# Performance work log

Measured on AMD Instinct MI355X. Metric: run time of the kernel, lower is better.

The kernel has to match this reference:

```python
import jax, jax.numpy as jnp
import numpy as np

N_NODES = 20000
N_EDGES = 320000
N_GRAPHS = 64


def gat_conv(x, src, dst, W, a_src, a_dst, bias, heads, ch, concat):
    # x: [N, F_in]; W: [F_in, heads*ch]; a_src/a_dst: [heads, ch]
    N = x.shape[0]
    h = (x @ W).reshape(N, heads, ch)                       # [N, H, C]
    alpha_s = jnp.sum(h * a_src, axis=-1)                   # [N, H]
    alpha_d = jnp.sum(h * a_dst, axis=-1)                   # [N, H]
    e = jax.nn.leaky_relu(alpha_s[src] + alpha_d[dst], 0.2) # [E, H]
    # segment softmax over incoming edges of each destination node
    m = jax.ops.segment_max(e, dst, num_segments=N)         # [N, H]
    ex = jnp.exp(e - m[dst])
    denom = jax.ops.segment_sum(ex, dst, num_segments=N)    # [N, H]
    alpha = ex / (denom[dst] + 1e-16)                       # [E, H]
    msg = h[src] * alpha[:, :, None]                        # [E, H, C]
    out = jax.ops.segment_sum(msg, dst, num_segments=N)     # [N, H, C]
    out = out.reshape(N, heads * ch) if concat else out.mean(axis=1)
    return out + bias, alpha


def setup_inputs() -> dict:
    key = jax.random.key(0)
    ks = jax.random.split(key, 24)
    dim_in, md, dim_out = 8, 64, 128
    hid = md * 4  # 256
    p = lambda k, shape: jax.random.normal(k, shape, dtype=jnp.float32) * 0.1
    inp = {
        "x_ppi": jax.random.normal(ks[0], (N_NODES, dim_in), dtype=jnp.float32),
        "ppi_edge_index": jax.random.randint(ks[1], (2, N_EDGES), 0, N_NODES),
        "ppi_batch": jnp.sort(jax.random.randint(ks[2], (N_NODES,), 0, N_GRAPHS)),
        # GATConv 1: dim_in -> 64, heads=4, concat
        "W1": p(ks[3], (dim_in, 4 * md)), "a_src1": p(ks[4], (4, md)), "a_dst1": p(ks[5], (4, md)), "b_gat1": jnp.zeros((hid,), jnp.float32),
        "lw1": p(ks[6], (dim_in, hid)), "lb1": jnp.zeros((hid,), jnp.float32),
        # GATConv 2: 256 -> 64, heads=4, concat
        "W2": p(ks[7], (hid, 4 * md)), "a_src2": p(ks[8], (4, md)), "a_dst2": p(ks[9], (4, md)), "b_gat2": jnp.zeros((hid,), jnp.float32),
        "lw2": p(ks[10], (hid, hid)), "lb2": jnp.zeros((hid,), jnp.float32),
        # GATConv 3: 256 -> 128, heads=6, concat=False (mean)
        "W3": p(ks[11], (hid, 6 * dim_out)), "a_src3": p(ks[12], (6, dim_out)), "a_dst3": p(ks[13], (6, dim_out)), "b_gat3": jnp.zeros((dim_out,), jnp.float32),
        "lw3": p(ks[14], (hid, dim_out)), "lb3": jnp.zeros((dim_out,), jnp.float32),
        # BatchNorm1d(dim_out), training-mode batch statistics
        "bn_gamma": jnp.ones((dim_out,), jnp.float32), "bn_beta": jnp.zeros((dim_out,), jnp.float32),
    }
    return inp


def reference(x_ppi, ppi_edge_index, ppi_batch,
              W1, a_src1, a_dst1, b_gat1, lw1, lb1,
              W2, a_src2, a_dst2, b_gat2, lw2, lb2,
              W3, a_src3, a_dst3, b_gat3, lw3, lb3,
              bn_gamma, bn_beta):
    src, dst = ppi_edge_index[0], ppi_edge_index[1]
    g1, _ = gat_conv(x_ppi, src, dst, W1, a_src1, a_dst1, b_gat1, heads=4, ch=64, concat=True)
    x = jax.nn.relu(g1 + x_ppi @ lw1 + lb1)
    g2, _ = gat_conv(x, src, dst, W2, a_src2, a_dst2, b_gat2, heads=4, ch=64, concat=True)
    x = jax.nn.relu(g2 + x @ lw2 + lb2)
    x_res = x @ lw3 + lb3
    g3, att = gat_conv(x, src, dst, W3, a_src3, a_dst3, b_gat3, heads=6, ch=128, concat=False)
    x = g3 + x_res
    x = jax.nn.relu(x)
    # BatchNorm1d, training mode (biased variance, eps=1e-5)
    mu = x.mean(axis=0)
    var = jnp.mean((x - mu) ** 2, axis=0)
    x = (x - mu) * jax.lax.rsqrt(var + 1e-5) * bn_gamma + bn_beta
    # global max pool over graphs
    pooled = jax.ops.segment_max(x, ppi_batch, num_segments=N_GRAPHS)
    return pooled, att
```

## Files before the change

### kernel.cpp

```cpp
#include <hip/hip_runtime.h>
#include <hip/hip_bf16.h>
#include <math.h>

#define N_NODES 20000
#define N_EDGES 320000
#define N_GRAPHS 64

typedef __bf16 bf16_t;
typedef bf16_t bf16x8 __attribute__((ext_vector_type(8)));
typedef bf16_t bf16x4 __attribute__((ext_vector_type(4)));
typedef bf16_t bf16x2 __attribute__((ext_vector_type(2)));
typedef float f32x4 __attribute__((ext_vector_type(4)));
typedef float f32x2 __attribute__((ext_vector_type(2)));

__global__ void hist_k(const int* __restrict__ dst, int* __restrict__ deg, int E) {
    int e = blockIdx.x * 256 + threadIdx.x;
    if (e < E) atomicAdd(&deg[dst[e]], 1);
}

__global__ __launch_bounds__(1024) void scan_k(const int* __restrict__ deg,
                                               int* __restrict__ offs,
                                               int* __restrict__ cursor, int n) {
    __shared__ int s_ws[16];
    int tid = threadIdx.x;
    int lane = tid & 63, w = tid >> 6;
    int carry = 0;
    for (int base = 0; base < n; base += 1024) {
        int i = base + tid;
        int v = (i < n) ? deg[i] : 0;
        int x = v;
        #pragma unroll
        for (int off = 1; off < 64; off <<= 1) {
            int t = __shfl_up(x, off);
            if (lane >= off) x += t;
        }
        if (lane == 63) s_ws[w] = x;
        __syncthreads();
        if (tid < 16) {
            int y = s_ws[tid];
            #pragma unroll
            for (int off = 1; off < 16; off <<= 1) {
                int t = __shfl_up(y, off);
                if (tid >= off) y += t;
            }
            s_ws[tid] = y;
        }
        __syncthreads();
        int wbase = (w > 0) ? s_ws[w - 1] : 0;
        int ex = carry + wbase + x - v;
        if (i < n) { offs[i] = ex; cursor[i] = ex; }
        carry += s_ws[15];
        __syncthreads();
    }
    if (tid == 0) offs[n] = carry;
}

__global__ void scatter_k(const int* __restrict__ src, const int* __restrict__ dst,
                          int* __restrict__ cursor, int* __restrict__ csr_src,
                          int* __restrict__ csr_eid, int E) {
    int e = blockIdx.x * 256 + threadIdx.x;
    if (e < E) {
        int d = dst[e];
        int p = atomicAdd(&cursor[d], 1);
        csr_src[p] = src[e];
        csr_eid[p] = e;
    }
}

__global__ __launch_bounds__(256) void wt_k(const float* __restrict__ W,
                                            bf16_t* __restrict__ Bt, int K, int N) {
    __shared__ float t[32][33];
    int k0 = blockIdx.y * 32, n0 = blockIdx.x * 32;
    int tx = threadIdx.x & 31, ty = threadIdx.x >> 5;
    for (int i = ty; i < 32; i += 8) t[i][tx] = W[(size_t)(k0 + i) * N + n0 + tx];
    __syncthreads();
    for (int i = ty; i < 32; i += 8)
        Bt[(size_t)(n0 + i) * K + k0 + tx] = (bf16_t)t[tx][i];
}

__global__ void w3s_k(const float* __restrict__ W3, const float* __restrict__ lw3,
                      bf16_t* __restrict__ Bt) {
    int id = blockIdx.x * 256 + threadIdx.x;
    if (id >= 128 * 1792) return;
    int n = id / 1792, k = id - n * 1792;
    float v;
    if (k < 1536) {
        int h = k >> 8, c = k & 255;
        v = W3[(size_t)c * 768 + h * 128 + n] * (1.f / 6.f);
    } else {
        int c = k - 1536;
        v = lw3[(size_t)c * 128 + n];
    }
    Bt[id] = (bf16_t)v;
}

__global__ void b40_k(const float* __restrict__ W1, const float* __restrict__ lw1,
                      float* __restrict__ B) {
    int id = blockIdx.x * 256 + threadIdx.x;
    if (id >= 40 * 256) return;
    int k = id >> 8, n = id & 255;
    float v;
    if (k < 32) {
        int h = k >> 3, c = k & 7;
        v = ((n >> 6) == h) ? W1[(size_t)c * 256 + n] : 0.f;
    } else {
        int c = k - 32;
        v = lw1[(size_t)c * 256 + n];
    }
    B[id] = v;
}

__global__ void va_k(const float* __restrict__ W, const float* __restrict__ a_s,
                     const float* __restrict__ a_d, float* __restrict__ Va,
                     float* __restrict__ Vd, int H, int C) {
    int k = blockIdx.x;
    int lane = threadIdx.x;
    const float* wr = W + (size_t)k * H * C;
    for (int h = 0; h < H; ++h) {
        float sa = 0.f, sd = 0.f;
        for (int c = lane; c < C; c += 64) {
            float wv = wr[h * C + c];
            sa += wv * a_s[h * C + c];
            sd += wv * a_d[h * C + c];
        }
        #pragma unroll
        for (int m = 32; m; m >>= 1) { sa += __shfl_xor(sa, m); sd += __shfl_xor(sd, m); }
        if (lane == 0) { Va[k * H + h] = sa; Vd[k * H + h] = sd; }
    }
}

__global__ void addb_k(const float* __restrict__ a, const float* __restrict__ b,
                       float* __restrict__ o, int n) {
    int i = blockIdx.x * 256 + threadIdx.x;
    if (i < n) o[i] = a[i] + b[i];
}

template <typename OUT>
__global__ __launch_bounds__(256) void gemm_k(const float* __restrict__ A,
                                              const float* __restrict__ B,
                                              OUT* __restrict__ C,
                                              const float* __restrict__ bias,
                                              int M, int N, int K, int relu) {
    __shared__ float As[16][65];
    __shared__ float Bs[16][64];
    int tid = threadIdx.x;
    int tx = tid & 15, ty = tid >> 4;
    int row0 = blockIdx.y * 64, col0 = blockIdx.x * 64;
    float acc[4][4] = {};
    for (int k0 = 0; k0 < K; k0 += 16) {
        #pragma unroll
        for (int i = 0; i < 4; ++i) {
            int idx = tid + i * 256;
            int m = idx >> 4, kk = idx & 15;
            int gm = row0 + m, gk = k0 + kk;
            As[kk][m] = (gm < M && gk < K) ? A[(size_t)gm * K + gk] : 0.f;
        }
        #pragma unroll
        for (int i = 0; i < 4; ++i) {
            int idx = tid + i * 256;
            int kk = idx >> 6, n = idx & 63;
            int gk = k0 + kk, gn = col0 + n;
            Bs[kk][n] = (gk < K && gn < N) ? B[(size_t)gk * N + gn] : 0.f;
        }
        __syncthreads();
        #pragma unroll
        for (int kk = 0; kk < 16; ++kk) {
            float a[4], b[4];
            #pragma unroll
            for (int i = 0; i < 4; ++i) a[i] = As[kk][ty * 4 + i];
            #pragma unroll
            for (int j = 0; j < 4; ++j) b[j] = Bs[kk][tx * 4 + j];
            #pragma unroll
            for (int i = 0; i < 4; ++i)
                #pragma unroll
                for (int j = 0; j < 4; ++j) acc[i][j] += a[i] * b[j];
        }
        __syncthreads();
    }
    #pragma unroll
    for (int i = 0; i < 4; ++i) {
        int gm = row0 + ty * 4 + i;
        if (gm >= M) continue;
        #pragma unroll
        for (int j = 0; j < 4; ++j) {
            int gn = col0 + tx * 4 + j;
            if (gn < N) {
                float r = acc[i][j] + (bias ? bias[gn] : 0.f);
                if (relu) r = fmaxf(r, 0.f);
                C[(size_t)gm * N + gn] = (OUT)r;
            }
        }
    }
}

template <typename OUT>
__global__ __launch_bounds__(256) void gemm_bf16_hn_k(
    const bf16_t* __restrict__ A, const bf16_t* __restrict__ Bt,
    OUT* __restrict__ C, const float* __restrict__ bias, int M, int N, int K,
    const float* __restrict__ asv, const float* __restrict__ adv,
    float* __restrict__ as_o, float* __restrict__ ad_o, int H) {
    __shared__ bf16_t As[128][40];
    __shared__ bf16_t Bs[64][40];
    int tid = threadIdx.x;
    int row0 = blockIdx.y * 128, col0 = blockIdx.x * 64;
    int wave = tid >> 6, lane = tid & 63, quad = lane >> 4, l16 = lane & 15;
    f32x4 acc[2][4] = {};
    int sr = tid >> 2;
    int sc = (tid & 3) * 8;
    for (int k0 = 0; k0 < K; k0 += 32) {
        #pragma unroll
        for (int half = 0; half < 2; ++half) {
            int r = sr + half * 64;
            int gm = row0 + r;
            bf16x8 v = {};
            if (gm < M) v = *(const bf16x8*)&A[(size_t)gm * K + k0 + sc];
            *(bf16x8*)&As[r][sc] = v;
        }
        {
            int gn = col0 + sr;
            bf16x8 w = {};
            if (gn < N) w = *(const bf16x8*)&Bt[(size_t)gn * K + k0 + sc];
            *(bf16x8*)&Bs[sr][sc] = w;
        }
        __syncthreads();
        bf16x8 af[2], bfr[4];
        #pragma unroll
        for (int i = 0; i < 2; ++i)
            af[i] = *(const bf16x8*)&As[wave * 32 + i * 16 + l16][quad * 8];
        #pragma unroll
        for (int j = 0; j < 4; ++j)
            bfr[j] = *(const bf16x8*)&Bs[j * 16 + l16][quad * 8];
        #pragma unroll
        for (int i = 0; i < 2; ++i)
            #pragma unroll
            for (int j = 0; j < 4; ++j)
                acc[i][j] = __builtin_amdgcn_mfma_f32_16x16x32_bf16(af[i], bfr[j],
                                                                   acc[i][j], 0, 0, 0);
        __syncthreads();
    }
    #pragma unroll
    for (int i = 0; i < 2; ++i) {
        int base_m = row0 + wave * 32 + i * 16 + quad * 4;
        #pragma unroll
        for (int j = 0; j < 4; ++j) {
            int gn = col0 + j * 16 + l16;
            float bv = bias ? bias[gn] : 0.f;
            #pragma unroll
            for (int r = 0; r < 4; ++r) {
                int gm = base_m + r;
                if (gm < M) C[(size_t)gm * N + gn] = (OUT)(acc[i][j][r] + bv);
            }
        }
    }
    if (asv) {
        int hd = col0 >> 6;
        float av[4], dv[4];
        #pragma unroll
        for (int j = 0; j < 4; ++j) {
            int ca = col0 + j * 16 + l16;
            av[j] = asv[ca];
            dv[j] = adv[ca];
        }
        #pragma unroll
        for (int i = 0; i < 2; ++i) {
            float sp[4] = {}, sd[4] = {};
            #pragma unroll
            for (int j = 0; j < 4; ++j)
                #pragma unroll
                for (int r = 0; r < 4; ++r) {
                    sp[r] += acc[i][j][r] * av[j];
                    sd[r] += acc[i][j][r] * dv[j];
                }
            #pragma unroll
            for (int m = 1; m < 16; m <<= 1)
                #pragma unroll
                for (int r = 0; r < 4; ++r) {
                    sp[r] += __shfl_xor(sp[r], m);
                    sd[r] += __shfl_xor(sd[r], m);
                }
            if (l16 == 0) {
                #pragma unroll
                for (int r = 0; r < 4; ++r) {
                    int gm = row0 + wave * 32 + i * 16 + quad * 4 + r;
                    if (gm < M) {
                        as_o[gm * H + hd] = sp[r];
                        ad_o[gm * H + hd] = sd[r];
                    }
                }
            }
        }
    }
}

__global__ __launch_bounds__(256) void gemm_bf16_thin_k(
    const bf16_t* __restrict__ A, const bf16_t* __restrict__ Bt,
    float* __restrict__ C, const float* __restrict__ bias, int M, int N, int K) {
    __shared__ bf16_t As[32][40];
    __shared__ bf16_t Bs[64][40];
    int tid = threadIdx.x;
    int row0 = blockIdx.y * 32, col0 = blockIdx.x * 64;
    int wave = tid >> 6, lane = tid & 63, quad = lane >> 4, l16 = lane & 15;
    int wr = wave & 1;
    int wc = wave >> 1;
    f32x4 acc[2] = {};
    int ar = tid >> 2, ac = (tid & 3) * 8;
    for (int k0 = 0; k0 < K; k0 += 32) {
        if (tid < 128) {
            int gm = row0 + ar;
            bf16x8 v = {};
            if (gm < M) v = *(const bf16x8*)&A[(size_t)gm * K + k0 + ac];
            *(bf16x8*)&As[ar][ac] = v;
        }
        *(bf16x8*)&Bs[ar][ac] = *(const bf16x8*)&Bt[(size_t)(col0 + ar) * K + k0 + ac];
        __syncthreads();
        bf16x8 af = *(const bf16x8*)&As[wr * 16 + l16][quad * 8];
        #pragma unroll
        for (int j = 0; j < 2; ++j) {
            bf16x8 bf = *(const bf16x8*)&Bs[wc * 32 + j * 16 + l16][quad * 8];
            acc[j] = __builtin_amdgcn_mfma_f32_16x16x32_bf16(af, bf, acc[j], 0, 0, 0);
        }
        __syncthreads();
    }
    #pragma unroll
    for (int j = 0; j < 2; ++j) {
        int gn = col0 + wc * 32 + j * 16 + l16;
        float bv = bias[gn];
        #pragma unroll
        for (int r = 0; r < 4; ++r) {
            int gm = row0 + wr * 16 + quad * 4 + r;
            if (gm < M) C[(size_t)gm * N + gn] = fmaxf(acc[j][r] + bv, 0.f);
        }
    }
}

__device__ __forceinline__ float leaky02(float v) { return v > 0.f ? v : 0.2f * v; }

__global__ void asad1_k(const float* __restrict__ x, const float* __restrict__ Va,
                        const float* __restrict__ Vd, float* __restrict__ as_,
                        float* __restrict__ ad_, int N) {
    int idx = blockIdx.x * 256 + threadIdx.x;
    if (idx >= N * 4) return;
    int j = idx >> 2, h = idx & 3;
    const float* xr = x + (size_t)j * 8;
    float sa = 0.f, sd = 0.f;
    #pragma unroll
    for (int c = 0; c < 8; ++c) {
        sa += xr[c] * Va[c * 4 + h];
        sd += xr[c] * Vd[c * 4 + h];
    }
    as_[idx] = sa;
    ad_[idx] = sd;
}

__global__ void asad3_k(const bf16_t* __restrict__ xb, const float* __restrict__ Va,
                        const float* __restrict__ Vd, float* __restrict__ as_,
                        float* __restrict__ ad_) {
    int j = blockIdx.x;
    int lane = threadIdx.x;
    bf16x4 v = *(const bf16x4*)&xb[(size_t)j * 256 + lane * 4];
    float sa[6] = {}, sd[6] = {};
    #pragma unroll
    for (int i = 0; i < 4; ++i) {
        int k = lane * 4 + i;
        float xv = (float)v[i];
        #pragma unroll
        for (int h = 0; h < 6; ++h) {
            sa[h] += xv * Va[k * 6 + h];
            sd[h] += xv * Vd[k * 6 + h];
        }
    }
    #pragma unroll
    for (int h = 0; h < 6; ++h) {
        float a = sa[h], d = sd[h];
        #pragma unroll
        for (int m = 32; m; m >>= 1) { a += __shfl_xor(a, m); d += __shfl_xor(d, m); }
        if (lane == 0) { as_[j * 6 + h] = a; ad_[j * 6 + h] = d; }
    }
}

__global__ __launch_bounds__(256) void agg_z1_k(
    const float* __restrict__ x, const float* __restrict__ as_,
    const float* __restrict__ ad_, const int* __restrict__ offs,
    const int* __restrict__ csr_src, float* __restrict__ z1) {
    int j = blockIdx.x * 4 + (threadIdx.x >> 6);
    int t = threadIdx.x & 63;
    int e_l = t >> 3, c = t & 7;
    int o0 = offs[j], deg = offs[j + 1] - o0;
    float adj0 = ad_[j * 4 + 0], adj1 = ad_[j * 4 + 1];
    float adj2 = ad_[j * 4 + 2], adj3 = ad_[j * 4 + 3];
    float acc[4] = {}, ws[4] = {};
    for (int e0 = 0; e0 < deg; e0 += 8) {
        int ne = min(8, deg - e0);
        if (e_l < ne) {
            int s = csr_src[o0 + e0 + e_l];
            float xv = x[(size_t)s * 8 + c];
            f32x4 a = *(const f32x4*)&as_[s * 4];
            float w0 = __expf(leaky02(a[0] + adj0));
            float w1 = __expf(leaky02(a[1] + adj1));
            float w2 = __expf(leaky02(a[2] + adj2));
            float w3 = __expf(leaky02(a[3] + adj3));
            acc[0] += w0 * xv; acc[1] += w1 * xv;
            acc[2] += w2 * xv; acc[3] += w3 * xv;
            ws[0] += w0; ws[1] += w1; ws[2] += w2; ws[3] += w3;
        }
    }
    #pragma unroll
    for (int m = 8; m < 64; m <<= 1)
        #pragma unroll
        for (int h = 0; h < 4; ++h) {
            acc[h] += __shfl_xor(acc[h], m);
            ws[h] += __shfl_xor(ws[h], m);
        }
    if (e_l == 0) {
        #pragma unroll
        for (int h = 0; h < 4; ++h)
            z1[(size_t)j * 40 + h * 8 + c] = acc[h] / (ws[h] + 1e-16f);
        z1[(size_t)j * 40 + 32 + c] = x[(size_t)j * 8 + c];
    }
}

__global__ __launch_bounds__(256) void agg_concat_k(
    const bf16_t* __restrict__ h, const float* __restrict__ as_,
    const float* __restrict__ ad_, const int* __restrict__ offs,
    const int* __restrict__ csr_src, const float* __restrict__ lin,
    const float* __restrict__ bgat, bf16_t* __restrict__ xb) {
    int j = blockIdx.x;
    int tid = threadIdx.x;
    int o0 = offs[j], deg = offs[j + 1] - o0;
    __shared__ int s_src[64];
    __shared__ float s_adj[4];
    __shared__ float s_ws[8][4];
    __shared__ float s_inv[4];
    __shared__ float s_red[8][256];
    if (tid < 4) s_adj[tid] = ad_[j * 4 + tid];
    int g = tid >> 5;
    int u = tid & 31;
    int myh = u >> 3;
    const char* hbase = (const char*)h + u * 16;
    f32x4 acc0 = {}, acc1 = {};
    float wsum = 0.f;
    for (int e0 = 0; e0 < deg; e0 += 64) {
        int ne = min(64, deg - e0);
        if (tid < ne) s_src[tid] = csr_src[o0 + e0 + tid];
        __syncthreads();
        float adj = s_adj[myh];
        #pragma unroll 2
        for (int e = g; e < ne; e += 8) {
            int s = s_src[e];
            float w = __expf(leaky02(as_[s * 4 + myh] + adj));
            bf16x8 v = *(const bf16x8*)(hbase + (size_t)s * 512);
            wsum += w;
            #pragma unroll
            for (int i = 0; i < 4; ++i) acc0[i] += w * (float)v[i];
            #pragma unroll
            for (int i = 0; i < 4; ++i) acc1[i] += w * (float)v[4 + i];
        }
        __syncthreads();
    }
    if ((u & 7) == 0) s_ws[g][myh] = wsum;
    *(f32x4*)&s_red[g][u * 8] = acc0;
    *(f32x4*)&s_red[g][u * 8 + 4] = acc1;
    __syncthreads();
    if (tid < 4) {
        float d = 0.f;
        #pragma unroll
        for (int g2 = 0; g2 < 8; ++g2) d += s_ws[g2][tid];
        s_inv[tid] = 1.f / (d + 1e-16f);
    }
    __syncthreads();
    {
        int c = tid;
        float s = 0.f;
        #pragma unroll
        for (int g2 = 0; g2 < 8; ++g2) s += s_red[g2][c];
        float v = fmaxf(s * s_inv[c >> 6] + bgat[c] + lin[(size_t)j * 256 + c], 0.f);
        xb[(size_t)j * 256 + c] = (bf16_t)v;
    }
}

__global__ __launch_bounds__(192) void agg_z3_k(
    const bf16_t* __restrict__ xb, const float* __restrict__ as_,
    const float* __restrict__ ad_, const int* __restrict__ offs,
    const int* __restrict__ csr_src, const int* __restrict__ csr_eid,
    bf16_t* __restrict__ z, float* __restrict__ att) {
    int j = blockIdx.x;
    int tid = threadIdx.x;
    int o0 = offs[j], deg = offs[j + 1] - o0;
    __shared__ float s_adj[6];
    __shared__ int s_src[64];
    __shared__ float s_w[64 * 6];
    __shared__ float s_inv[6];
    if (tid < 6) s_adj[tid] = ad_[j * 6 + tid];
    __syncthreads();
    int h = tid >> 5;
    int c = tid & 31;
    const char* xbase = (const char*)xb + c * 16;
    f32x4 a0 = {}, a1 = {};
    float wsum = 0.f;
    for (int e0 = 0; e0 < deg; e0 += 64) {
        int ne = min(64, deg - e0);
        #pragma unroll
        for (int base = 0; base < 2; ++base) {
            int idx = tid + base * 192;
            if (idx < ne * 6) {
                int e = idx / 6, hh = idx - e * 6;
                int s = csr_src[o0 + e0 + e];
                if (hh == 0) s_src[e] = s;
                s_w[idx] = __expf(leaky02(as_[s * 6 + hh] + s_adj[hh]));
            }
        }
        __syncthreads();
        #pragma unroll 4
        for (int e = 0; e < ne; ++e) {
            int s = s_src[e];
            float w = s_w[e * 6 + h];
            bf16x8 v = *(const bf16x8*)(xbase + (size_t)s * 512);
            wsum += w;
            #pragma unroll
            for (int i = 0; i < 4; ++i) a0[i] += w * (float)v[i];
            #pragma unroll
            for (int i = 0; i < 4; ++i) a1[i] += w * (float)v[4 + i];
        }
        __syncthreads();
    }
    float inv = 1.f / (wsum + 1e-16f);
    {
        bf16x8 o;
        #pragma unroll
        for (int i = 0; i < 4; ++i) o[i] = (bf16_t)(a0[i] * inv);
        #pragma unroll
        for (int i = 0; i < 4; ++i) o[4 + i] = (bf16_t)(a1[i] * inv);
        *(bf16x8*)&z[(size_t)j * 1792 + h * 256 + c * 8] = o;
    }
    if (tid < 32)
        *(bf16x8*)&z[(size_t)j * 1792 + 1536 + tid * 8] =
            *(const bf16x8*)&xb[(size_t)j * 256 + tid * 8];
    if (c == 0) s_inv[h] = inv;
    __syncthreads();
    for (int idx = tid; idx < deg * 6; idx += 192) {
        int e = idx / 6, hh = idx - e * 6;
        int p = o0 + e;
        int s = csr_src[p];
        att[(size_t)csr_eid[p] * 6 + hh] =
            __expf(leaky02(as_[s * 6 + hh] + s_adj[hh])) * s_inv[hh];
    }
}

__global__ void bn_stats_k(const float* __restrict__ y, float* __restrict__ sums, int N) {
    int c = threadIdx.x;
    float s = 0.f, q = 0.f;
    for (int r = blockIdx.x; r < N; r += gridDim.x) {
        float v = y[(size_t)r * 128 + c];
        s += v;
        q += v * v;
    }
    atomicAdd(&sums[c], s);
    atomicAdd(&sums[128 + c], q);
}
__global__ void bn_scale_k(const float* __restrict__ sums, const float* __restrict__ gamma,
                           const float* __restrict__ beta, float* __restrict__ scale,
                           float* __restrict__ shift, int N) {
    int c = threadIdx.x;
    float mu = sums[c] / (float)N;
    float var = fmaxf(sums[128 + c] / (float)N - mu * mu, 0.f);
    float inv = rsqrtf(var + 1e-5f) * gamma[c];
    scale[c] = inv;
    shift[c] = beta[c] - mu * inv;
}

__device__ __forceinline__ unsigned f2key(float f) {
    unsigned b = __float_as_uint(f);
    return (b & 0x80000000u) ? ~b : (b | 0x80000000u);
}
__global__ void pool_init_k(unsigned* __restrict__ pool_u) {
    int i = blockIdx.x * 256 + threadIdx.x;
    if (i < N_GRAPHS * 128) pool_u[i] = f2key(-3.402823466e38f * 2.0f);
}
__global__ void norm_pool_k(const float* __restrict__ y, const float* __restrict__ scale,
                            const float* __restrict__ shift, const int* __restrict__ batch,
                            unsigned* __restrict__ pool_u, int N) {
    int idx = blockIdx.x * 256 + threadIdx.x;
    if (idx >= N * 128) return;
    int n = idx >> 7, c = idx & 127;
    float v = y[idx] * scale[c] + shift[c];
    atomicMax(&pool_u[batch[n] * 128 + c], f2key(v));
}
__global__ void pool_write_k(const unsigned* __restrict__ pool_u, float* __restrict__ out) {
    int i = blockIdx.x * 256 + threadIdx.x;
    if (i < N_GRAPHS * 128) {
        unsigned u = pool_u[i];
        unsigned b = (u & 0x80000000u) ? (u & 0x7FFFFFFFu) : ~u;
        out[i] = __uint_as_float(b);
    }
}

extern "C" void kernel_launch(void* const* d_in, const int* in_sizes, int n_in,
                              void* d_out, int out_size, void* d_ws, size_t ws_size,
                              hipStream_t stream) {
    const int N = N_NODES, E = N_EDGES;
    const float* x_ppi = (const float*)d_in[0];
    const int* edge = (const int*)d_in[1];
    const int* batch = (const int*)d_in[2];
    const float* W1 = (const float*)d_in[3];
    const float* a_src1 = (const float*)d_in[4];
    const float* a_dst1 = (const float*)d_in[5];
    const float* b_gat1 = (const float*)d_in[6];
    const float* lw1 = (const float*)d_in[7];
    const float* lb1 = (const float*)d_in[8];
    const float* W2 = (const float*)d_in[9];
    const float* a_src2 = (const float*)d_in[10];
    const float* a_dst2 = (const float*)d_in[11];
    const float* b_gat2 = (const float*)d_in[12];
    const float* lw2 = (const float*)d_in[13];
    const float* lb2 = (const float*)d_in[14];
    const float* W3 = (const float*)d_in[15];
    const float* a_src3 = (const float*)d_in[16];
    const float* a_dst3 = (const float*)d_in[17];
    const float* b_gat3 = (const float*)d_in[18];
    const float* lw3 = (const float*)d_in[19];
    const float* lb3 = (const float*)d_in[20];
    const float* bn_gamma = (const float*)d_in[21];
    const float* bn_beta = (const float*)d_in[22];

    const int* src = edge;
    const int* dst = edge + E;

    size_t off = 0;
    auto alloc = [&](size_t bytes) {
        size_t o = off;
        off = (off + bytes + 255) & ~(size_t)255;
        return o;
    };
    char* ws = (char*)d_ws;
    bf16_t* xb = (bf16_t*)(ws + alloc((size_t)N * 256 * 2));
    bf16_t* zbig = (bf16_t*)(ws + alloc((size_t)N * 1792 * 2));
    bf16_t* hb = zbig;
    bf16_t* z3 = zbig;
    float* lin = (float*)(ws + alloc((size_t)N * 256 * 4));
    float* z1 = (float*)(ws + alloc((size_t)N * 40 * 4));
    float* as_ = (float*)(ws + alloc((size_t)N * 6 * 4));
    float* ad_ = (float*)(ws + alloc((size_t)N * 6 * 4));
    int* deg = (int*)(ws + alloc((size_t)(N + 1) * 4));
    int* offs = (int*)(ws + alloc((size_t)(N + 1) * 4));
    int* cursor = (int*)(ws + alloc((size_t)(N + 1) * 4));
    int* csr_src = (int*)(ws + alloc((size_t)E * 4));
    int* csr_eid = (int*)(ws + alloc((size_t)E * 4));
    bf16_t* Wt2 = (bf16_t*)(ws + alloc((size_t)256 * 256 * 2));
    bf16_t* lwt2 = (bf16_t*)(ws + alloc((size_t)256 * 256 * 2));
    bf16_t* Bt3s = (bf16_t*)(ws + alloc((size_t)128 * 1792 * 2));
    float* B40 = (float*)(ws + alloc((size_t)40 * 256 * 4));
    float* Va1 = (float*)(ws + alloc(8 * 4 * 4));
    float* Vd1 = (float*)(ws + alloc(8 * 4 * 4));
    float* Va3 = (float*)(ws + alloc(256 * 6 * 4));
    float* Vd3 = (float*)(ws + alloc(256 * 6 * 4));
    float* bias1s = (float*)(ws + alloc(256 * 4));
    float* bias3s = (float*)(ws + alloc(128 * 4));
    float* bn_sums = (float*)(ws + alloc(256 * 4));
    float* bn_scale = (float*)(ws + alloc(128 * 4));
    float* bn_shift = (float*)(ws + alloc(128 * 4));
    unsigned* pool_u = (unsigned*)(ws + alloc((size_t)N_GRAPHS * 128 * 4));

    float* out_pool = (float*)d_out;
    float* out_att = (float*)d_out + N_GRAPHS * 128;

    hipMemsetAsync(deg, 0, (size_t)N * 4, stream);
    hist_k<<<(E + 255) / 256, 256, 0, stream>>>(dst, deg, E);
    scan_k<<<1, 1024, 0, stream>>>(deg, offs, cursor, N);
    scatter_k<<<(E + 255) / 256, 256, 0, stream>>>(src, dst, cursor, csr_src, csr_eid, E);
    wt_k<<<dim3(8, 8), 256, 0, stream>>>(W2, Wt2, 256, 256);
    wt_k<<<dim3(8, 8), 256, 0, stream>>>(lw2, lwt2, 256, 256);
    w3s_k<<<896, 256, 0, stream>>>(W3, lw3, Bt3s);
    b40_k<<<40, 256, 0, stream>>>(W1, lw1, B40);
    va_k<<<8, 64, 0, stream>>>(W1, a_src1, a_dst1, Va1, Vd1, 4, 64);
    va_k<<<256, 64, 0, stream>>>(W3, a_src3, a_dst3, Va3, Vd3, 6, 128);
    addb_k<<<1, 256, 0, stream>>>(lb1, b_gat1, bias1s, 256);
    addb_k<<<1, 128, 0, stream>>>(lb3, b_gat3, bias3s, 128);

    asad1_k<<<(N * 4 + 255) / 256, 256, 0, stream>>>(x_ppi, Va1, Vd1, as_, ad_, N);
    agg_z1_k<<<N / 4, 256, 0, stream>>>(x_ppi, as_, ad_, offs, csr_src, z1);
    gemm_k<bf16_t><<<dim3(4, 313), 256, 0, stream>>>(z1, B40, xb, bias1s, N, 256, 40, 1);

    gemm_bf16_hn_k<bf16_t><<<dim3(4, 157), 256, 0, stream>>>(xb, Wt2, hb, nullptr, N, 256, 256,
                                                             a_src2, a_dst2, as_, ad_, 4);
    gemm_bf16_hn_k<float><<<dim3(4, 157), 256, 0, stream>>>(xb, lwt2, lin, lb2, N, 256, 256,
                                                            nullptr, nullptr, nullptr, nullptr,
                                                            0);
    agg_concat_k<<<N, 256, 0, stream>>>(hb, as_, ad_, offs, csr_src, lin, b_gat2, xb);

    float* y = lin;
    asad3_k<<<N, 64, 0, stream>>>(xb, Va3, Vd3, as_, ad_);
    agg_z3_k<<<N, 192, 0, stream>>>(xb, as_, ad_, offs, csr_src, csr_eid, z3, out_att);
    gemm_bf16_thin_k<<<dim3(2, 625), 256, 0, stream>>>(z3, Bt3s, y, bias3s, N, 128, 1792);

    hipMemsetAsync(bn_sums, 0, 256 * 4, stream);
    bn_stats_k<<<160, 128, 0, stream>>>(y, bn_sums, N);
    bn_scale_k<<<1, 128, 0, stream>>>(bn_sums, bn_gamma, bn_beta, bn_scale, bn_shift, N);

    pool_init_k<<<(N_GRAPHS * 128 + 255) / 256, 256, 0, stream>>>(pool_u);
    norm_pool_k<<<((size_t)N * 128 + 255) / 256, 256, 0, stream>>>(y, bn_scale, bn_shift, batch,
                                                                   pool_u, N);
    pool_write_k<<<(N_GRAPHS * 128 + 255) / 256, 256, 0, stream>>>(pool_u, out_pool);
}
```

Baseline: 457.4 us.

## Restructure layer-3 aggregation: one wavefront per node, stage neighbor features once in LDS

The layer-3 aggregation kernel moves from 192 threads (one 32-lane group per head, each reloading the neighbor row) to a single 64-thread wavefront. Each neighbor's 256-wide bf16 row is loaded once, converted to fp32 into LDS in chunks of 8 edges, and every thread accumulates all 6 heads for 4 channels. This removes the 6x redundant global gathers of the same source row across heads. It costs smaller blocks, more registers per thread (24 accumulators), more barriers per edge chunk and a rotated LDS store pattern.

```diff
diff --git a/kernel.cpp b/kernel.cpp
--- a/kernel.cpp
+++ b/kernel.cpp
@@ -478,70 +478,91 @@
     }
 }
 
-__global__ __launch_bounds__(192) void agg_z3_k(
+__global__ __launch_bounds__(64) void agg_z3_k(
     const bf16_t* __restrict__ xb, const float* __restrict__ as_,
     const float* __restrict__ ad_, const int* __restrict__ offs,
     const int* __restrict__ csr_src, const int* __restrict__ csr_eid,
     bf16_t* __restrict__ z, float* __restrict__ att) {
     int j = blockIdx.x;
-    int tid = threadIdx.x;
+    int t = threadIdx.x;
     int o0 = offs[j], deg = offs[j + 1] - o0;
-    __shared__ float s_adj[6];
-    __shared__ int s_src[64];
-    __shared__ float s_w[64 * 6];
-    __shared__ float s_inv[6];
-    if (tid < 6) s_adj[tid] = ad_[j * 6 + tid];
+    __shared__ float s_adj[6], s_inv[6];
+    __shared__ float s_w[8 * 6];
+    __shared__ float s_wp[48];
+    __shared__ float s_xf[8][260];
+    if (t < 6) s_adj[t] = ad_[j * 6 + t];
     __syncthreads();
-    int h = tid >> 5;
-    int c = tid & 31;
-    const char* xbase = (const char*)xb + c * 16;
-    f32x4 a0 = {}, a1 = {};
-    float wsum = 0.f;
-    for (int e0 = 0; e0 < deg; e0 += 64) {
-        int ne = min(64, deg - e0);
-        #pragma unroll
-        for (int base = 0; base < 2; ++base) {
-            int idx = tid + base * 192;
-            if (idx < ne * 6) {
-                int e = idx / 6, hh = idx - e * 6;
+    int we = t / 6, wh = t - we * 6;
+    int p = t & 15;
+    int eb = t >> 4;
+    float wrun = 0.f;
+    float acc[6][4] = {};
+    for (int e0 = 0; e0 < deg; e0 += 8) {
+        int ne = min(8, deg - e0);
+        if (t < 48 && we < ne) {
+            int s = csr_src[o0 + e0 + we];
+            float w = __expf(leaky02(as_[s * 6 + wh] + s_adj[wh]));
+            s_w[we * 6 + wh] = w;
+            wrun += w;
+        }
+        #pragma unroll
+        for (int half = 0; half < 2; ++half) {
+            int e = eb + half * 4;
+            if (e < ne) {
                 int s = csr_src[o0 + e0 + e];
-                if (hh == 0) s_src[e] = s;
-                s_w[idx] = __expf(leaky02(as_[s * 6 + hh] + s_adj[hh]));
+                float cv[16];
+                #pragma unroll
+                for (int b = 0; b < 2; ++b) {
+                    bf16x8 v = *(const bf16x8*)&xb[(size_t)s * 256 + p * 16 + b * 8];
+                    #pragma unroll
+                    for (int q = 0; q < 8; ++q) cv[b * 8 + q] = (float)v[q];
+                }
+                #pragma unroll
+                for (int qq = 0; qq < 4; ++qq) {
+                    int q = (qq + (p >> 1)) & 3;
+                    f32x4 w4 = {cv[q * 4], cv[q * 4 + 1], cv[q * 4 + 2], cv[q * 4 + 3]};
+                    *(f32x4*)&s_xf[e][p * 16 + q * 4] = w4;
+                }
             }
         }
         __syncthreads();
-        #pragma unroll 4
         for (int e = 0; e < ne; ++e) {
-            int s = s_src[e];
-            float w = s_w[e * 6 + h];
-            bf16x8 v = *(const bf16x8*)(xbase + (size_t)s * 512);
-            wsum += w;
-            #pragma unroll
-            for (int i = 0; i < 4; ++i) a0[i] += w * (float)v[i];
-            #pragma unroll
-            for (int i = 0; i < 4; ++i) a1[i] += w * (float)v[4 + i];
-        }
-        __syncthreads();
-    }
-    float inv = 1.f / (wsum + 1e-16f);
-    {
-        bf16x8 o;
-        #pragma unroll
-        for (int i = 0; i < 4; ++i) o[i] = (bf16_t)(a0[i] * inv);
-        #pragma unroll
-        for (int i = 0; i < 4; ++i) o[4 + i] = (bf16_t)(a1[i] * inv);
-        *(bf16x8*)&z[(size_t)j * 1792 + h * 256 + c * 8] = o;
-    }
-    if (tid < 32)
-        *(bf16x8*)&z[(size_t)j * 1792 + 1536 + tid * 8] =
-            *(const bf16x8*)&xb[(size_t)j * 256 + tid * 8];
-    if (c == 0) s_inv[h] = inv;
+            f32x4 x4 = *(const f32x4*)&s_xf[e][t * 4];
+            const f32x2* wp2 = (const f32x2*)&s_w[e * 6];
+            f32x2 w01 = wp2[0], w23 = wp2[1], w45 = wp2[2];
+            float wv[6] = {w01[0], w01[1], w23[0], w23[1], w45[0], w45[1]};
+            #pragma unroll
+            for (int h = 0; h < 6; ++h)
+                #pragma unroll
+                for (int i = 0; i < 4; ++i) acc[h][i] += wv[h] * x4[i];
+        }
+        __syncthreads();
+    }
+    if (t < 48) s_wp[t] = wrun;
     __syncthreads();
-    for (int idx = tid; idx < deg * 6; idx += 192) {
+    if (t < 6) {
+        float d = 0.f;
+        #pragma unroll
+        for (int k = 0; k < 8; ++k) d += s_wp[k * 6 + t];
+        s_inv[t] = 1.f / (d + 1e-16f);
+    }
+    __syncthreads();
+    #pragma unroll
+    for (int h = 0; h < 6; ++h) {
+        float inv = s_inv[h];
+        bf16x4 o;
+        #pragma unroll
+        for (int i = 0; i < 4; ++i) o[i] = (bf16_t)(acc[h][i] * inv);
+        *(bf16x4*)&z[(size_t)j * 1792 + h * 256 + t * 4] = o;
+    }
+    if (t < 32)
+        *(bf16x8*)&z[(size_t)j * 1792 + 1536 + t * 8] =
+            *(const bf16x8*)&xb[(size_t)j * 256 + t * 8];
+    for (int idx = t; idx < deg * 6; idx += 64) {
         int e = idx / 6, hh = idx - e * 6;
-        int p = o0 + e;
-        int s = csr_src[p];
-        att[(size_t)csr_eid[p] * 6 + hh] =
+        int pp = o0 + e;
+        int s = csr_src[pp];
+        att[(size_t)csr_eid[pp] * 6 + hh] =
             __expf(leaky02(as_[s * 6 + hh] + s_adj[hh])) * s_inv[hh];
     }
 }
@@ -689,7 +710,7 @@
 
     float* y = lin;
     asad3_k<<<N, 64, 0, stream>>>(xb, Va3, Vd3, as_, ad_);
-    agg_z3_k<<<N, 192, 0, stream>>>(xb, as_, ad_, offs, csr_src, csr_eid, z3, out_att);
+    agg_z3_k<<<N, 64, 0, stream>>>(xb, as_, ad_, offs, csr_src, csr_eid, z3, out_att);
     gemm_bf16_thin_k<<<dim3(2, 625), 256, 0, stream>>>(z3, Bt3s, y, bias3s, N, 128, 1792);
 
     hipMemsetAsync(bn_sums, 0, 256 * 4, stream);
```

Result: slower. 501.2 us (+9.6%).
